# Performance work log

Hardware: AMD Instinct MI355X
Metric: run time of the kernel (lower is better)

Reference implementation:

```python
import jax, jax.numpy as jnp
import numpy as np

DIM = 256
N_CHANNELS = 8
NEIGHBORS = 16


def setup_inputs() -> dict:
    key = jax.random.key(0)
    kx, kw = jax.random.split(key)
    B, N, D = 4, 1024, DIM
    x = jax.random.normal(kx, (B, N, D), dtype=jnp.float32)
    # nn.Linear(dim, dim*2*n_channels, bias=False); store as [in, out] so y = x @ W
    W_qk = jax.random.normal(kw, (D, 2 * N_CHANNELS * D), dtype=jnp.float32) * (D ** -0.5)
    return {"x": x, "W_qk": W_qk}


def _norm_edge(edge):
    # edge: [B, C, N, N]
    norm_row = edge / (edge.sum(axis=-1, keepdims=True) + 1e-6)
    norm_col = norm_row / (norm_row.sum(axis=-2, keepdims=True) + 1e-6)
    # norm_row @ norm_col^T
    return jnp.einsum('bcnk,bcmk->bcnm', norm_row, norm_col)


def reference(x, W_qk):
    B, N, D = x.shape
    C = N_CHANNELS
    scale = D ** -0.5
    qk = (x @ W_qk).reshape(B, N, 2, C, D)
    q = jnp.transpose(qk[:, :, 0], (0, 2, 1, 3))  # [B, C, N, D]
    k = jnp.transpose(qk[:, :, 1], (0, 2, 1, 3))  # [B, C, N, D]
    attn = jax.nn.softmax(jnp.einsum('bcnd,bcmd->bcnm', q, k) * scale, axis=-1)

    # clip(): top-k neighbor mask from channel-summed (detached) attention
    sum_edge = jax.lax.stop_gradient(attn).sum(axis=1)  # [B, N, N]
    kk = min(NEIGHBORS, N)
    _, top_idx = jax.lax.top_k(sum_edge, kk)  # [B, N, kk]
    b_idx = jnp.arange(B)[:, None, None]
    r_idx = jnp.arange(N)[None, :, None]
    mask = jnp.zeros((B, N, N), dtype=attn.dtype).at[b_idx, r_idx, top_idx].set(1.0)
    mask = jnp.maximum(mask, jnp.eye(N, dtype=attn.dtype))  # identity diag
    edge = mask[:, None] * attn  # [B, C, N, N]
    return _norm_edge(edge)
```

## Files before the change

### kernel.cpp

```cpp
#include <hip/hip_runtime.h>
#include <hip/hip_bf16.h>
#include <math.h>

#define BB 4
#define NN 1024
#define DD 256
#define CC 8
#define KNBR 16
#define MAXSEL 17
#define ZCAP (NN * MAXSEL)

typedef _Float16 f16x8_t __attribute__((ext_vector_type(8)));
typedef _Float16 f16x4_t __attribute__((ext_vector_type(4)));
typedef float    f32x4_t __attribute__((ext_vector_type(4)));

__device__ __forceinline__ void gl2lds16(const _Float16* g, _Float16* ldsbase) {
    __builtin_amdgcn_global_load_lds(
        (const __attribute__((address_space(1))) unsigned int*)g,
        (__attribute__((address_space(3))) unsigned int*)ldsbase, 16, 0, 0);
}

__device__ __forceinline__ void split2(float v, _Float16& h, _Float16& l) {
    h = (_Float16)v;
    l = (_Float16)(v - (float)h);
}

__global__ __launch_bounds__(256) void split_all(const float* __restrict__ x,
                                                 const float* __restrict__ W,
                                                 _Float16* __restrict__ xh,
                                                 _Float16* __restrict__ xl,
                                                 _Float16* __restrict__ Wth,
                                                 _Float16* __restrict__ Wtl,
                                                 int* __restrict__ countb) {
    const int tid = threadIdx.x;
    if (blockIdx.x < 1024) {
        int i = (blockIdx.x * 256 + tid) * 4;
        float4 v = *(const float4*)(x + i);
        f16x4_t hv, lv;
        _Float16 h, l;
        split2(v.x, h, l); hv[0] = h; lv[0] = l;
        split2(v.y, h, l); hv[1] = h; lv[1] = l;
        split2(v.z, h, l); hv[2] = h; lv[2] = l;
        split2(v.w, h, l); hv[3] = h; lv[3] = l;
        *(f16x4_t*)(xh + i) = hv;
        *(f16x4_t*)(xl + i) = lv;
    } else {
        const int b2 = blockIdx.x - 1024;
        if (b2 == 0) {
            int4 zz = make_int4(0, 0, 0, 0);
#pragma unroll
            for (int g = 0; g < 4; g++) ((int4*)countb)[tid + 256 * g] = zz;
        }
        __shared__ float t[64][65];
        const int n0 = (b2 & 63) * 64;
        const int k0 = (b2 >> 6) * 64;
#pragma unroll
        for (int i = 0; i < 16; i++) {
            int k = i * 4 + (tid >> 6);
            int n = tid & 63;
            t[k][n] = W[(size_t)(k0 + k) * 4096 + n0 + n];
        }
        __syncthreads();
#pragma unroll
        for (int i = 0; i < 16; i++) {
            int n = i * 4 + (tid >> 6);
            int k = tid & 63;
            _Float16 h, l;
            split2(t[k][n] * 16.f, h, l);
            size_t o = (size_t)(n0 + n) * 256 + k0 + k;
            Wth[o] = h; Wtl[o] = l;
        }
    }
}

#define STG(dst, src, rowbase, kk)                                             \
    do {                                                                       \
        gl2lds16((src) + (size_t)((rowbase) + r_st) * 256 + (kk) + c8,         \
                 &(dst)[(w * 64) * 8]);                                        \
        gl2lds16((src) + (size_t)((rowbase) + 64 + r_st) * 256 + (kk) + c8,    \
                 &(dst)[(256 + w * 64) * 8]);                                  \
    } while (0)

#define MFMA3(accv, AH, AL, BH, BL)                                            \
    do {                                                                       \
        accv = __builtin_amdgcn_mfma_f32_16x16x32_f16(AL, BH, accv, 0, 0, 0);  \
        accv = __builtin_amdgcn_mfma_f32_16x16x32_f16(AH, BL, accv, 0, 0, 0);  \
        accv = __builtin_amdgcn_mfma_f32_16x16x32_f16(AH, BH, accv, 0, 0, 0);  \
    } while (0)

#define COMPUTE(AH, AL, BH, BL)                                                \
    do {                                                                       \
        f16x8_t ah[4], al[4];                                                  \
        _Pragma("unroll")                                                      \
        for (int mi = 0; mi < 4; mi++) {                                       \
            int r = (wr * 64 + mi * 16 + lm) * 32 + qx8;                       \
            ah[mi] = *(const f16x8_t*)&(AH)[r];                                \
            al[mi] = *(const f16x8_t*)&(AL)[r];                                \
        }                                                                      \
        _Pragma("unroll")                                                      \
        for (int ni = 0; ni < 4; ni++) {                                       \
            int rb = (wc * 64 + ni * 16 + lm) * 32 + qx8;                      \
            f16x8_t bh = *(const f16x8_t*)&(BH)[rb];                           \
            f16x8_t bl = *(const f16x8_t*)&(BL)[rb];                           \
            _Pragma("unroll")                                                  \
            for (int mi = 0; mi < 4; mi++)                                     \
                MFMA3(acc[mi][ni], ah[mi], al[mi], bh, bl);                    \
        }                                                                      \
    } while (0)

__global__ __launch_bounds__(256) void gemm_xw_mfma(
        const _Float16* __restrict__ xh, const _Float16* __restrict__ xl,
        const _Float16* __restrict__ wth, const _Float16* __restrict__ wtl,
        _Float16* __restrict__ qh, _Float16* __restrict__ ql,
        _Float16* __restrict__ kh, _Float16* __restrict__ kl) {
    __shared__ __align__(16) char smem[65536];
    _Float16* Ah0 = (_Float16*)smem;
    _Float16* Al0 = (_Float16*)(smem + 8192);
    _Float16* Bh0 = (_Float16*)(smem + 16384);
    _Float16* Bl0 = (_Float16*)(smem + 24576);
    _Float16* Ah1 = (_Float16*)(smem + 32768);
    _Float16* Al1 = (_Float16*)(smem + 40960);
    _Float16* Bh1 = (_Float16*)(smem + 49152);
    _Float16* Bl1 = (_Float16*)(smem + 57344);
    const int tid = threadIdx.x, lane = tid & 63, w = tid >> 6;
    const int wr = w >> 1, wc = w & 1;
    const int lm = lane & 15, quad = lane >> 4;
    const int row0 = blockIdx.y * 128, col0 = blockIdx.x * 128;
    const int r_st = tid >> 2;
    const int c8 = (((tid & 3) ^ ((tid >> 3) & 3)) * 8);
    const int qx8 = ((quad ^ ((lm >> 1) & 3)) * 8);

    f32x4_t acc[4][4];
#pragma unroll
    for (int i = 0; i < 4; i++)
#pragma unroll
        for (int j = 0; j < 4; j++) acc[i][j] = (f32x4_t)(0.f);

    STG(Ah0, xh, row0, 0); STG(Al0, xl, row0, 0);
    STG(Bh0, wth, col0, 0); STG(Bl0, wtl, col0, 0);
    __syncthreads();
#pragma unroll
    for (int t = 0; t < 8; t += 2) {
        {
            int kn = (t + 1) * 32;
            if (t + 1 < 8) {
                STG(Ah1, xh, row0, kn); STG(Al1, xl, row0, kn);
                STG(Bh1, wth, col0, kn); STG(Bl1, wtl, col0, kn);
            }
            COMPUTE(Ah0, Al0, Bh0, Bl0);
            __syncthreads();
        }
        {
            int kn = (t + 2) * 32;
            if (t + 2 < 8) {
                STG(Ah0, xh, row0, kn); STG(Al0, xl, row0, kn);
                STG(Bh0, wth, col0, kn); STG(Bl0, wtl, col0, kn);
            }
            COMPUTE(Ah1, Al1, Bh1, Bl1);
            __syncthreads();
        }
    }

    float* tr = (float*)smem;
    const int s = col0 >> 11, c = (col0 >> 8) & 7, dbase = col0 & 255;
    _Float16* dh = s ? kh : qh;
    _Float16* dl = s ? kl : ql;
    const int rl = tid >> 2;
    const int cb = (tid & 3) * 8;
#pragma unroll
    for (int p = 0; p < 2; p++) {
        if (p) __syncthreads();
        if (wr == p) {
#pragma unroll
            for (int mi = 0; mi < 4; mi++) {
                int rloc = mi * 16 + quad * 4;
#pragma unroll
                for (int ni = 0; ni < 4; ni++) {
                    int cl = wc * 64 + ni * 16 + lm;
#pragma unroll
                    for (int r = 0; r < 4; r++)
                        tr[(rloc + r) * 132 + cl] = acc[mi][ni][r];
                }
            }
        }
        __syncthreads();
        int rr = row0 + p * 64 + rl;
        int bb = rr >> 10, n = rr & 1023;
        size_t base = (((size_t)(bb * CC + c)) * NN + n) * DD + dbase;
#pragma unroll
        for (int g = 0; g < 4; g++) {
            int ccol = g * 32 + cb;
            f16x8_t hv, lv;
#pragma unroll
            for (int e = 0; e < 8; e++) {
                float vv = tr[rl * 132 + ccol + e];
                _Float16 h, l;
                split2(vv, h, l);
                hv[e] = h; lv[e] = l;
            }
            *(f16x8_t*)(dh + base + ccol) = hv;
            *(f16x8_t*)(dl + base + ccol) = lv;
        }
    }
}

__global__ __launch_bounds__(256) void gemm_qkt_mfma(
        const _Float16* __restrict__ qh, const _Float16* __restrict__ ql,
        const _Float16* __restrict__ kh, const _Float16* __restrict__ kl,
        float* __restrict__ attn) {
    __shared__ __align__(16) char smem[65536];
    _Float16* Ah0 = (_Float16*)smem;
    _Float16* Al0 = (_Float16*)(smem + 8192);
    _Float16* Bh0 = (_Float16*)(smem + 16384);
    _Float16* Bl0 = (_Float16*)(smem + 24576);
    _Float16* Ah1 = (_Float16*)(smem + 32768);
    _Float16* Al1 = (_Float16*)(smem + 40960);
    _Float16* Bh1 = (_Float16*)(smem + 49152);
    _Float16* Bl1 = (_Float16*)(smem + 57344);
    const int tid = threadIdx.x, lane = tid & 63, w = tid >> 6;
    const int wr = w >> 1, wc = w & 1;
    const int lm = lane & 15, quad = lane >> 4;
    const int id = blockIdx.x;
    const int rb8 = id & 7, qq = id >> 3;
    const int j = qq & 63, zhi = qq >> 6;
    const int z = zhi * 8 + rb8;
    const int row0 = (j >> 3) * 128, col0 = (j & 7) * 128;
    const size_t zo = (size_t)z * NN * DD;
    float* Cm = attn + (size_t)z * NN * NN;
    const int r_st = tid >> 2;
    const int c8 = (((tid & 3) ^ ((tid >> 3) & 3)) * 8);
    const int qx8 = ((quad ^ ((lm >> 1) & 3)) * 8);
    const float scale = 0.0625f / 256.0f;

    f32x4_t acc[4][4];
#pragma unroll
    for (int i = 0; i < 4; i++)
#pragma unroll
        for (int j2 = 0; j2 < 4; j2++) acc[i][j2] = (f32x4_t)(0.f);

    const _Float16* qhz = qh + zo;
    const _Float16* qlz = ql + zo;
    const _Float16* khz = kh + zo;
    const _Float16* klz = kl + zo;

    STG(Ah0, qhz, row0, 0); STG(Al0, qlz, row0, 0);
    STG(Bh0, khz, col0, 0); STG(Bl0, klz, col0, 0);
    __syncthreads();
#pragma unroll
    for (int t = 0; t < 8; t += 2) {
        {
            int kn = (t + 1) * 32;
            if (t + 1 < 8) {
                STG(Ah1, qhz, row0, kn); STG(Al1, qlz, row0, kn);
                STG(Bh1, khz, col0, kn); STG(Bl1, klz, col0, kn);
            }
            COMPUTE(Ah0, Al0, Bh0, Bl0);
            __syncthreads();
        }
        {
            int kn = (t + 2) * 32;
            if (t + 2 < 8) {
                STG(Ah0, qhz, row0, kn); STG(Al0, qlz, row0, kn);
                STG(Bh0, khz, col0, kn); STG(Bl0, klz, col0, kn);
            }
            COMPUTE(Ah1, Al1, Bh1, Bl1);
            __syncthreads();
        }
    }

#pragma unroll
    for (int mi = 0; mi < 4; mi++)
#pragma unroll
        for (int ni = 0; ni < 4; ni++) {
            int row = row0 + wr * 64 + mi * 16 + quad * 4;
            int col = col0 + wc * 64 + ni * 16 + lm;
#pragma unroll
            for (int r = 0; r < 4; r++)
                Cm[(size_t)(row + r) * NN + col] = acc[mi][ni][r] * scale;
        }
}

__global__ __launch_bounds__(256) void softmax_topk(const float* __restrict__ attn,
                                                    float2* __restrict__ ml,
                                                    int* __restrict__ idx,
                                                    int* __restrict__ cnt,
                                                    int* __restrict__ countb,
                                                    float* __restrict__ colsum) {
    __shared__ float psum[4][NN];
    __shared__ float cval[64];
    __shared__ int   cidx[64];
    __shared__ int fsel[MAXSEL];
    __shared__ int fcnt;
    const int bn = blockIdx.x, b = bn >> 10, n = bn & 1023;
    const int tid = threadIdx.x, lane = tid & 63, w = tid >> 6;

    if (tid < CC) colsum[(size_t)(b * CC + tid) * NN + n] = 0.f;

    const int colb = lane * 16;
    float4 u[2][4];
#pragma unroll
    for (int p = 0; p < 2; p++) {
        const int c = w * 2 + p;
        const float* rowp = attn + (((size_t)(b * CC + c) * NN + n) * NN) + colb;
#pragma unroll
        for (int g = 0; g < 4; g++) u[p][g] = *(const float4*)(rowp + g * 4);
    }

    float acc[16];
#pragma unroll
    for (int e = 0; e < 16; e++) acc[e] = 0.f;

#pragma unroll
    for (int p = 0; p < 2; p++) {
        const int c = w * 2 + p;
        const float* f = (const float*)&u[p][0];
        float mx = f[0];
#pragma unroll
        for (int e = 1; e < 16; e++) mx = fmaxf(mx, f[e]);
#pragma unroll
        for (int off = 1; off < 64; off <<= 1) mx = fmaxf(mx, __shfl_xor(mx, off));
        float sm = 0.f;
        float pe[16];
#pragma unroll
        for (int e = 0; e < 16; e++) { pe[e] = expf(f[e] - mx); sm += pe[e]; }
#pragma unroll
        for (int off = 1; off < 64; off <<= 1) sm += __shfl_xor(sm, off);
        if (lane == 0) ml[(size_t)(b * CC + c) * NN + n] = make_float2(mx, sm);
        float inv = 1.0f / sm;
#pragma unroll
        for (int e = 0; e < 16; e++) acc[e] += pe[e] * inv;
    }
#pragma unroll
    for (int g = 0; g < 4; g++)
        *(float4*)&psum[w][colb + g * 4] =
            make_float4(acc[g * 4], acc[g * 4 + 1], acc[g * 4 + 2], acc[g * 4 + 3]);
    __syncthreads();

    const int m4 = tid * 4;
    float4 a0 = *(const float4*)&psum[0][m4];
    float4 a1 = *(const float4*)&psum[1][m4];
    float4 a2 = *(const float4*)&psum[2][m4];
    float4 a3 = *(const float4*)&psum[3][m4];
    float v0 = a0.x + a1.x + a2.x + a3.x;
    float v1 = a0.y + a1.y + a2.y + a3.y;
    float v2 = a0.z + a1.z + a2.z + a3.z;
    float v3 = a0.w + a1.w + a2.w + a3.w;

    float myv = 0.f; int myi = 0;
    for (int it = 0; it < KNBR; it++) {
        float bv = v0; int bi = m4;
        if (v1 > bv) { bv = v1; bi = m4 + 1; }
        if (v2 > bv) { bv = v2; bi = m4 + 2; }
        if (v3 > bv) { bv = v3; bi = m4 + 3; }
#pragma unroll
        for (int off = 1; off < 64; off <<= 1) {
            float ov = __shfl_xor(bv, off);
            int oi = __shfl_xor(bi, off);
            if (ov > bv || (ov == bv && oi < bi)) { bv = ov; bi = oi; }
        }
        if (lane == it) { myv = bv; myi = bi; }
        v0 = (bi == m4)     ? -INFINITY : v0;
        v1 = (bi == m4 + 1) ? -INFINITY : v1;
        v2 = (bi == m4 + 2) ? -INFINITY : v2;
        v3 = (bi == m4 + 3) ? -INFINITY : v3;
    }
    if (lane < KNBR) { cval[w * KNBR + lane] = myv; cidx[w * KNBR + lane] = myi; }
    __syncthreads();

    if (w == 0) {
        float mv = cval[lane]; int mi = cidx[lane];
        for (int it = 0; it < KNBR; it++) {
            float bv = mv; int bi = mi;
#pragma unroll
            for (int off = 1; off < 64; off <<= 1) {
                float ov = __shfl_xor(bv, off);
                int oi = __shfl_xor(bi, off);
                if (ov > bv || (ov == bv && oi < bi)) { bv = ov; bi = oi; }
            }
            if (lane == 0) fsel[it] = bi;
            if (mi == bi) mv = -INFINITY;
        }
        if (lane == 0) {
            bool has = false;
            for (int t = 0; t < KNBR; t++)
                if (fsel[t] == n) has = true;
            int c = KNBR;
            if (!has) { fsel[KNBR] = n; c = KNBR + 1; }
            fcnt = c;
            cnt[bn] = c;
        }
    }
    __syncthreads();
    if (tid < fcnt) {
        idx[bn * MAXSEL + tid] = fsel[tid];
        atomicAdd(&countb[b * NN + fsel[tid]], 1);
    }
}

__global__ __launch_bounds__(256) void scan_offb(const int* __restrict__ countb,
                                                 int* __restrict__ offb,
                                                 int* __restrict__ curs) {
    __shared__ int wtot[4];
    const int b = blockIdx.x, tid = threadIdx.x, lane = tid & 63, w = tid >> 6;
    int c0 = countb[b * NN + tid * 4 + 0];
    int c1 = countb[b * NN + tid * 4 + 1];
    int c2 = countb[b * NN + tid * 4 + 2];
    int c3 = countb[b * NN + tid * 4 + 3];
    int tsum = c0 + c1 + c2 + c3;
    int incl = tsum;
#pragma unroll
    for (int off = 1; off < 64; off <<= 1) {
        int v = __shfl_up(incl, off);
        if (lane >= off) incl += v;
    }
    if (lane == 63) wtot[w] = incl;
    __syncthreads();
    int woff = 0;
    for (int i = 0; i < w; i++) woff += wtot[i];
    int base = woff + incl - tsum;
    int o0 = base, o1 = base + c0, o2 = base + c0 + c1, o3 = base + c0 + c1 + c2;
    offb[b * NN + tid * 4 + 0] = o0;
    offb[b * NN + tid * 4 + 1] = o1;
    offb[b * NN + tid * 4 + 2] = o2;
    offb[b * NN + tid * 4 + 3] = o3;
#pragma unroll
    for (int c = 0; c < CC; c++) {
        int z = b * CC + c;
        curs[z * NN + tid * 4 + 0] = o0;
        curs[z * NN + tid * 4 + 1] = o1;
        curs[z * NN + tid * 4 + 2] = o2;
        curs[z * NN + tid * 4 + 3] = o3;
    }
}

__global__ __launch_bounds__(256) void rownorm_fill(const float* __restrict__ attn,
                                                    const float2* __restrict__ ml,
                                                    const int* __restrict__ idx,
                                                    const int* __restrict__ cnt,
                                                    int* __restrict__ curs,
                                                    float* __restrict__ nr,
                                                    float* __restrict__ colsum,
                                                    int* __restrict__ eidx,
                                                    float* __restrict__ eval) {
    const int t = blockIdx.x * 256 + threadIdx.x;
    const int z = t >> 10, n = t & 1023;
    const int b = z >> 3;
    const int bn = b * NN + n;
    const int c_ = cnt[bn];
    const float* arow = attn + (size_t)t * NN;
    const float2 MM = ml[t];
    const float invl = 1.0f / MM.y;
    const size_t zb = (size_t)z * ZCAP;
    float a[MAXSEL];
    int kk[MAXSEL];
    float s = 0.f;
#pragma unroll
    for (int j = 0; j < MAXSEL; j++) {
        if (j < c_) {
            kk[j] = idx[bn * MAXSEL + j];
            float p = expf(arow[kk[j]] - MM.x) * invl;
            a[j] = p; s += p;
        }
    }
    const float inv = 1.f / (s + 1e-6f);
#pragma unroll
    for (int j = 0; j < MAXSEL; j++) {
        if (j < c_) {
            float v = a[j] * inv;
            nr[(size_t)t * MAXSEL + j] = v;
            atomicAdd(&colsum[(size_t)z * NN + kk[j]], v);
            int p = atomicAdd(&curs[z * NN + kk[j]], 1);
            eidx[zb + p] = n;
            eval[zb + p] = v;
        }
    }
}

__global__ __launch_bounds__(256) void out_sparse(const float* __restrict__ nr,
                                                  const int* __restrict__ idx,
                                                  const int* __restrict__ cnt,
                                                  const int* __restrict__ offb,
                                                  const int* __restrict__ countb,
                                                  const float* __restrict__ colsum,
                                                  const int* __restrict__ eidx,
                                                  const float* __restrict__ eval,
                                                  float* __restrict__ out) {
    __shared__ float row[4][NN];
    __shared__ float gscale[4][MAXSEL];
    __shared__ int   goff[4][MAXSEL];
    __shared__ int   gpref[4][MAXSEL + 1];
    const int tid = threadIdx.x, lane = tid & 63, w = tid >> 6;
    const int t = blockIdx.x * 4 + w;
    const int z = t >> 10;
    const int b = z >> 3;
    const int bn = b * NN + (t & 1023);
    const size_t zb = (size_t)z * ZCAP;

    f32x4_t zz = (f32x4_t)(0.f);
#pragma unroll
    for (int q = 0; q < 4; q++) ((f32x4_t*)row[w])[q * 64 + lane] = zz;

    const int c_ = cnt[bn];
    float sc = 0.f;
    int off = 0, len = 0;
    if (lane < c_) {
        int k = idx[bn * MAXSEL + lane];
        float wgt = nr[(size_t)t * MAXSEL + lane];
        sc = wgt / (colsum[(size_t)z * NN + k] + 1e-6f);
        off = offb[b * NN + k];
        len = countb[b * NN + k];
    }
    int incl = len;
#pragma unroll
    for (int o = 1; o < 32; o <<= 1) {
        int v = __shfl_up(incl, o);
        if (lane >= o) incl += v;
    }
    if (lane < MAXSEL) { gscale[w][lane] = sc; goff[w][lane] = off; }
    if (lane <= MAXSEL) gpref[w][lane] = incl - len;
    __syncthreads();

    const int tot = gpref[w][MAXSEL];
    for (int e = lane; e < tot; e += 64) {
        int lo = 0, hi = MAXSEL;
        while (hi - lo > 1) {
            int mid = (lo + hi) >> 1;
            if (gpref[w][mid] <= e) lo = mid; else hi = mid;
        }
        int i = e - gpref[w][lo] + goff[w][lo];
        int m = eidx[zb + i];
        float v = eval[zb + i];
        atomicAdd(&row[w][m], gscale[w][lo] * v);
    }
    __syncthreads();

    const size_t ob = (size_t)t * NN;
    f32x4_t* op = (f32x4_t*)(out + ob);
#pragma unroll
    for (int q = 0; q < 4; q++) {
        f32x4_t vo = ((f32x4_t*)row[w])[q * 64 + lane];
        __builtin_nontemporal_store(vo, op + q * 64 + lane);
    }
}

extern "C" void kernel_launch(void* const* d_in, const int* in_sizes, int n_in,
                              void* d_out, int out_size, void* d_ws, size_t ws_size,
                              hipStream_t stream) {
    const float* x = (const float*)d_in[0];
    const float* W = (const float*)d_in[1];
    float* out = (float*)d_out;
    char* ws = (char*)d_ws;

    float* attn = (float*)d_out;

    _Float16* qh  = (_Float16*)(ws);
    _Float16* ql  = (_Float16*)(ws + 16777216ull);
    _Float16* kh  = (_Float16*)(ws + 33554432ull);
    _Float16* kl  = (_Float16*)(ws + 50331648ull);
    _Float16* xh  = (_Float16*)(ws + 67108864ull);
    _Float16* xl  = (_Float16*)(ws + 69206016ull);
    _Float16* wth = (_Float16*)(ws + 71303168ull);
    _Float16* wtl = (_Float16*)(ws + 73400320ull);
    int*    idx  = (int*)   (ws + 75497472ull);
    int*    cnt  = (int*)   (ws + 75776000ull);
    float*  nr   = (float*) (ws + 75792384ull);
    float*  colsum = (float*)(ws + 78020608ull);
    float2* ml   = (float2*)(ws + 78151680ull);
    int*    countb = (int*) (ws + 78413824ull);
    int*    offb = (int*)   (ws + 78430208ull);
    int*    curs = (int*)   (ws + 78446592ull);
    int*    eidx = (int*)   (ws + 78577664ull);
    float*  eval = (float*) (ws + 80805888ull);

    split_all<<<1280, 256, 0, stream>>>(x, W, xh, xl, wth, wtl, countb);
    gemm_xw_mfma<<<dim3(32, 32), 256, 0, stream>>>(xh, xl, wth, wtl,
                                                   qh, ql, kh, kl);
    gemm_qkt_mfma<<<2048, 256, 0, stream>>>(qh, ql, kh, kl, attn);
    softmax_topk<<<4096, 256, 0, stream>>>(attn, ml, idx, cnt, countb, colsum);
    scan_offb<<<4, 256, 0, stream>>>(countb, offb, curs);
    rownorm_fill<<<128, 256, 0, stream>>>(attn, ml, idx, cnt, curs, nr, colsum,
                                          eidx, eval);
    out_sparse<<<8192, 256, 0, stream>>>(nr, idx, cnt, offb, countb, colsum,
                                         eidx, eval, out);
}
```

Before: 421.3 us.

## Replace iterative top-k shuffle reductions with radix bisection on float bits

```diff
diff --git a/kernel.cpp b/kernel.cpp
--- a/kernel.cpp
+++ b/kernel.cpp
@@ -286,9 +286,7 @@
                                                     int* __restrict__ cnt,
                                                     int* __restrict__ countb,
                                                     float* __restrict__ colsum) {
-    __shared__ float psum[4][NN];
-    __shared__ float cval[64];
-    __shared__ int   cidx[64];
+    __shared__ float psum[4][1280];
     __shared__ int fsel[MAXSEL];
     __shared__ int fcnt;
     const int bn = blockIdx.x, b = bn >> 10, n = bn & 1023;
@@ -297,6 +295,7 @@
     if (tid < CC) colsum[(size_t)(b * CC + tid) * NN + n] = 0.f;
 
     const int colb = lane * 16;
+    const int pb   = lane * 20;
     float4 u[2][4];
 #pragma unroll
     for (int p = 0; p < 2; p++) {
@@ -332,58 +331,77 @@
     }
 #pragma unroll
     for (int g = 0; g < 4; g++)
-        *(float4*)&psum[w][colb + g * 4] =
+        *(float4*)&psum[w][pb + g * 4] =
             make_float4(acc[g * 4], acc[g * 4 + 1], acc[g * 4 + 2], acc[g * 4 + 3]);
     __syncthreads();
 
-    const int m4 = tid * 4;
-    float4 a0 = *(const float4*)&psum[0][m4];
-    float4 a1 = *(const float4*)&psum[1][m4];
-    float4 a2 = *(const float4*)&psum[2][m4];
-    float4 a3 = *(const float4*)&psum[3][m4];
-    float v0 = a0.x + a1.x + a2.x + a3.x;
-    float v1 = a0.y + a1.y + a2.y + a3.y;
-    float v2 = a0.z + a1.z + a2.z + a3.z;
-    float v3 = a0.w + a1.w + a2.w + a3.w;
-
-    float myv = 0.f; int myi = 0;
-    for (int it = 0; it < KNBR; it++) {
-        float bv = v0; int bi = m4;
-        if (v1 > bv) { bv = v1; bi = m4 + 1; }
-        if (v2 > bv) { bv = v2; bi = m4 + 2; }
-        if (v3 > bv) { bv = v3; bi = m4 + 3; }
-#pragma unroll
-        for (int off = 1; off < 64; off <<= 1) {
-            float ov = __shfl_xor(bv, off);
-            int oi = __shfl_xor(bi, off);
-            if (ov > bv || (ov == bv && oi < bi)) { bv = ov; bi = oi; }
-        }
-        if (lane == it) { myv = bv; myi = bi; }
-        v0 = (bi == m4)     ? -INFINITY : v0;
-        v1 = (bi == m4 + 1) ? -INFINITY : v1;
-        v2 = (bi == m4 + 2) ? -INFINITY : v2;
-        v3 = (bi == m4 + 3) ? -INFINITY : v3;
-    }
-    if (lane < KNBR) { cval[w * KNBR + lane] = myv; cidx[w * KNBR + lane] = myi; }
+    const int p4 = tid * 4 + (tid >> 2) * 4;
+    float4 a0 = *(const float4*)&psum[0][p4];
+    float4 a1 = *(const float4*)&psum[1][p4];
+    float4 a2 = *(const float4*)&psum[2][p4];
+    float4 a3 = *(const float4*)&psum[3][p4];
+    float4 vs;
+    vs.x = a0.x + a1.x + a2.x + a3.x;
+    vs.y = a0.y + a1.y + a2.y + a3.y;
+    vs.z = a0.z + a1.z + a2.z + a3.z;
+    vs.w = a0.w + a1.w + a2.w + a3.w;
+    *(float4*)&psum[0][p4] = vs;
     __syncthreads();
 
     if (w == 0) {
-        float mv = cval[lane]; int mi = cidx[lane];
-        for (int it = 0; it < KNBR; it++) {
-            float bv = mv; int bi = mi;
-#pragma unroll
-            for (int off = 1; off < 64; off <<= 1) {
-                float ov = __shfl_xor(bv, off);
-                int oi = __shfl_xor(bi, off);
-                if (ov > bv || (ov == bv && oi < bi)) { bv = ov; bi = oi; }
+        unsigned vb[16];
+#pragma unroll
+        for (int g = 0; g < 4; g++) {
+            float4 t4 = *(const float4*)&psum[0][pb + g * 4];
+            vb[g * 4 + 0] = __float_as_uint(t4.x);
+            vb[g * 4 + 1] = __float_as_uint(t4.y);
+            vb[g * 4 + 2] = __float_as_uint(t4.z);
+            vb[g * 4 + 3] = __float_as_uint(t4.w);
+        }
+        unsigned lo = 0u, hi = 0x7F800000u;
+        while (lo < hi) {
+            unsigned mid = lo + ((hi - lo) >> 1);
+            int c = 0;
+#pragma unroll
+            for (int e = 0; e < 16; e++)
+                c += (int)__popcll(__ballot(vb[e] > mid));
+            if (c <= 15) hi = mid; else lo = mid + 1;
+        }
+        const unsigned V = hi;
+        int cgt = 0, ceq = 0;
+#pragma unroll
+        for (int e = 0; e < 16; e++) {
+            cgt += (vb[e] > V) ? 1 : 0;
+            ceq += (vb[e] == V) ? 1 : 0;
+        }
+        int pk = cgt | (ceq << 16);
+        int incl = pk;
+#pragma unroll
+        for (int o = 1; o < 64; o <<= 1) {
+            int v2 = __shfl_up(incl, o);
+            if (lane >= o) incl += v2;
+        }
+        int tot = __shfl(incl, 63);
+        int c1 = tot & 0xffff;
+        int need = KNBR - c1;
+        int excl = incl - pk;
+        int pg = excl & 0xffff;
+        int pe2 = excl >> 16;
+        int lg = 0, le = 0;
+#pragma unroll
+        for (int e = 0; e < 16; e++) {
+            if (vb[e] > V) {
+                fsel[pg + lg] = colb + e; lg++;
+            } else if (vb[e] == V) {
+                if (pe2 + le < need) fsel[c1 + pe2 + le] = colb + e;
+                le++;
             }
-            if (lane == 0) fsel[it] = bi;
-            if (mi == bi) mv = -INFINITY;
         }
         if (lane == 0) {
             bool has = false;
-            for (int t = 0; t < KNBR; t++)
-                if (fsel[t] == n) has = true;
+#pragma unroll
+            for (int t2 = 0; t2 < KNBR; t2++)
+                if (fsel[t2] == n) has = true;
             int c = KNBR;
             if (!has) { fsel[KNBR] = n; c = KNBR + 1; }
             fcnt = c;
@@ -538,8 +556,7 @@
     f32x4_t* op = (f32x4_t*)(out + ob);
 #pragma unroll
     for (int q = 0; q < 4; q++) {
-        f32x4_t vo = ((f32x4_t*)row[w])[q * 64 + lane];
-        __builtin_nontemporal_store(vo, op + q * 64 + lane);
+        op[q * 64 + lane] = ((f32x4_t*)row[w])[q * 64 + lane];
     }
 }
 
```

Result: faster. 389.2 us (-7.6%).
